# Performance work log

Measured on AMD Instinct MI355X. Metric: run time of the kernel, lower is better.

## Reference

```python
import jax, jax.numpy as jnp
from jax import lax
import numpy as np


def _conv(x, w, stride):
    # x: [B,C,D,H,W], w: [3,3,3,Cin,Cout]; kernel 3, pad 1 (matches SubMConv3d / SparseConv3d(3, s, padding=1))
    return lax.conv_general_dilated(x, w, (stride, stride, stride), [(1, 1)] * 3,
                                    dimension_numbers=('NCDHW', 'DHWIO', 'NCDHW'))


def _bn_relu(y, scale, shift, mask):
    # eval-mode BatchNorm folded to scale/shift, ReLU, then restrict to active sites
    return jnp.maximum(y * scale[None, :, None, None, None] + shift[None, :, None, None, None], 0.0) * mask


def _downsample_mask(m):
    # SparseConv3d(k=3, s=2, p=1): output site active iff any input in its 3x3x3 window is active
    return lax.reduce_window(m, -jnp.inf, lax.max, (1, 1, 3, 3, 3), (1, 1, 2, 2, 2),
                             [(0, 0), (0, 0), (1, 1), (1, 1), (1, 1)])


def setup_inputs() -> dict:
    key = jax.random.key(0)
    ks = jax.random.split(key, 40)
    B, D = 1, 128
    occ = jax.random.uniform(ks[0], (B, 1, D, D, D)) < 0.05
    x = jax.random.normal(ks[1], (B, 16, D, D, D), jnp.float32) * occ

    def w(k, ci, co):
        return jax.random.normal(k, (3, 3, 3, ci, co), jnp.float32) * (1.0 / np.sqrt(27.0 * ci))

    def sc(k, c):
        return jax.random.uniform(k, (c,), jnp.float32, 0.5, 1.5)

    def sh(k, c):
        return jax.random.normal(k, (c,), jnp.float32) * 0.1

    chans = [(16, 16), (16, 16), (16, 32), (32, 32), (32, 32), (32, 64), (64, 64), (64, 64), (64, 64)]
    names = ['w0a', 'w0b', 'wd0', 'w1a', 'w1b', 'wd1', 'w2a', 'w2b', 'w2c']
    d = {'x': x, 'mask': occ}
    i = 2
    for n, (ci, co) in zip(names, chans):
        d[n] = w(ks[i], ci, co)
        d['s' + n[1:]] = sc(ks[i + 1], co)
        d['b' + n[1:]] = sh(ks[i + 2], co)
        i += 3
    return d


def reference(x, mask, w0a, s0a, b0a, w0b, s0b, b0b, wd0, sd0, bd0,
              w1a, s1a, b1a, w1b, s1b, b1b, wd1, sd1, bd1,
              w2a, s2a, b2a, w2b, s2b, b2b, w2c, s2c, b2c):
    m0 = mask.astype(x.dtype)                       # active sites at full res [B,1,128,128,128]
    h = _bn_relu(_conv(x, w0a, 1), s0a, b0a, m0)    # conv0 (subm0)
    h = _bn_relu(_conv(h, w0b, 1), s0b, b0b, m0)
    m1 = _downsample_mask(m0)                       # down0 activity [B,1,64,64,64]
    h = _bn_relu(_conv(h, wd0, 2), sd0, bd0, m1)
    h = _bn_relu(_conv(h, w1a, 1), s1a, b1a, m1)    # conv1 (subm1)
    h = _bn_relu(_conv(h, w1b, 1), s1b, b1b, m1)
    m2 = _downsample_mask(m1)                       # down1 activity [B,1,32,32,32]
    h = _bn_relu(_conv(h, wd1, 2), sd1, bd1, m2)
    h = _bn_relu(_conv(h, w2a, 1), s2a, b2a, m2)    # conv2 (subm2)
    h = _bn_relu(_conv(h, w2b, 1), s2b, b2b, m2)
    h = _bn_relu(_conv(h, w2c, 1), s2c, b2c, m2)
    return h                                        # .dense() -> [B,64,32,32,32]
```

## Files before the change

### kernel.cpp

```cpp
#include <hip/hip_runtime.h>
#include <cstdint>

typedef unsigned short u16;
typedef unsigned int u32;
typedef unsigned char u8;
typedef unsigned long long u64;
typedef __attribute__((ext_vector_type(8))) short short8;
typedef __attribute__((ext_vector_type(4))) float f32x4;

#define CAP 131072

__device__ __forceinline__ float bf1(u16 v){ union{u32 i; float f;} c; c.i = ((u32)v) << 16; return c.f; }
__device__ __forceinline__ u16 f2bf(float f){
    union{float f; u32 i;} c; c.f = f; u32 i = c.i;
    return (u16)((i + 0x7FFFu + ((i >> 16) & 1u)) >> 16);
}

constexpr int ilog2c(int n){ return n <= 1 ? 0 : 1 + ilog2c(n / 2); }

struct P18 { const void* p[18]; };
struct PJobs {
    const void* src[9];
    u32 start[10];
    int cin[9], cout[9], mode[9];
};

__global__ void detect_k(const u16* __restrict__ s0a, u32* __restrict__ flag){
    if (threadIdx.x == 0){
        int ok = 1;
        #pragma unroll
        for (int i = 0; i < 8; i += 2){
            u16 v = s0a[i];
            if (v < 0x3F00u || v > 0x3FC0u) ok = 0;
        }
        flag[0] = ok ? 1u : 0u;
    }
}

__global__ __launch_bounds__(256)
void prep_k(PJobs J, u16* __restrict__ FR, const u32* __restrict__ flag){
    const int gi = blockIdx.x * 256 + threadIdx.x;
    if (gi >= (int)J.start[9]) return;
    int j = 0;
    while (gi >= (int)J.start[j + 1]) ++j;
    const int i = gi - (int)J.start[j];
    const void* w = J.src[j];
    const int CIN = J.cin[j], COUT = J.cout[j];
    const int jj = i & 7;
    const int lane = (i >> 3) & 63;
    int rest = i >> 9;
    int src = -1;
    if (J.mode[j] == 0){
        const int KC = CIN >> 5, NT = COUT >> 4;
        const int nt = rest % NT; rest /= NT;
        const int kc = rest % KC; const int tap = rest / KC;
        const int k = kc * 32 + (lane >> 4) * 8 + jj;
        const int co = nt * 16 + (lane & 15);
        src = (tap * CIN + k) * COUT + co;
    } else if (J.mode[j] == 1){
        const int nt = rest & 1; const int pair = rest >> 1;
        const int kg = (lane >> 4) * 8 + jj;
        const int tap = pair * 2 + (kg >> 4);
        const int ci = kg & 15;
        const int co = nt * 16 + (lane & 15);
        if (tap < 27) src = (tap * 16 + ci) * 32 + co;
    } else {
        const int pair = rest;
        const int kg = (lane >> 4) * 8 + jj;
        const int tap = pair * 2 + (kg >> 4);
        const int ci = kg & 15;
        const int co = lane & 15;
        if (tap < 27) src = (tap * 16 + ci) * 16 + co;
    }
    float v = 0.f;
    if (src >= 0) v = flag[0] ? bf1(((const u16*)w)[src]) : ((const float*)w)[src];
    FR[gi] = f2bf(v);
}

__global__ __launch_bounds__(64)
void scales_k(P18 ps, float* __restrict__ S, const u32* __restrict__ flag){
    const int b = blockIdx.x, t = threadIdx.x;
    const int len[18] = {16,16,16,16,32,32,32,32,32,32,64,64,64,64,64,64,64,64};
    const int off[18] = {0,16,32,48,64,96,128,160,192,224,256,320,384,448,512,576,640,704};
    if (t < len[b]){
        const float v = flag[0] ? bf1(((const u16*)ps.p[b])[t]) : ((const float*)ps.p[b])[t];
        S[off[b] + t] = v;
    }
}

__global__ __launch_bounds__(256)
void actmask_k(const void* __restrict__ xv, u64* __restrict__ bmask,
               u32* __restrict__ bcnt, const u32* __restrict__ flag){
    const int v = blockIdx.x * 256 + threadIdx.x;
    const size_t N = 2097152;
    u32 a = 0;
    if (flag[0]) {
        const u16* x = (const u16*)xv;
        #pragma unroll
        for (int c = 0; c < 16; ++c) a |= (u32)(x[(size_t)c * N + v]) & 0x7FFFu;
    } else {
        const u32* x = (const u32*)xv;
        #pragma unroll
        for (int c = 0; c < 16; ++c) a |= x[(size_t)c * N + v] & 0x7FFFFFFFu;
    }
    const u64 m = __ballot(a != 0);
    __shared__ u32 wc[4];
    const int lane = threadIdx.x & 63, wv = threadIdx.x >> 6;
    if (lane == 0) { bmask[v >> 6] = m; wc[wv] = (u32)__popcll(m); }
    __syncthreads();
    if (threadIdx.x == 0) bcnt[blockIdx.x] = wc[0] + wc[1] + wc[2] + wc[3];
}

__global__ __launch_bounds__(1024)
void scan_k(const u32* __restrict__ bcnt, u32* __restrict__ boff, u32* __restrict__ cnt){
    __shared__ u32 lds[1024];
    const int t = threadIdx.x;
    u32 loc[8]; u32 s = 0;
    #pragma unroll
    for (int i = 0; i < 8; ++i){ loc[i] = s; s += bcnt[t * 8 + i]; }
    lds[t] = s;
    __syncthreads();
    u32 v = s;
    for (int d = 1; d < 1024; d <<= 1){
        u32 o = (t >= d) ? lds[t - d] : 0;
        __syncthreads();
        v += o; lds[t] = v;
        __syncthreads();
    }
    const u32 base = v - s;
    #pragma unroll
    for (int i = 0; i < 8; ++i) boff[t * 8 + i] = base + loc[i];
    if (t == 1023) cnt[0] = v;
}

__global__ __launch_bounds__(256)
void scatter2_k(const void* __restrict__ xv, const u64* __restrict__ bmask,
                const u32* __restrict__ boff, int* __restrict__ idxmap,
                int* __restrict__ alist, u16* __restrict__ f,
                const u32* __restrict__ flag){
    const int v = blockIdx.x * 256 + threadIdx.x;
    const int lane = threadIdx.x & 63, wv = threadIdx.x >> 6;
    const u64 m = bmask[v >> 6];
    __shared__ u32 wc[4];
    if (lane == 0) wc[wv] = (u32)__popcll(m);
    __syncthreads();
    u32 wbase = 0;
    for (int i = 0; i < wv; ++i) wbase += wc[i];
    const bool act = (m >> lane) & 1ull;
    const u32 rank = (u32)__popcll(m & ((1ull << lane) - 1ull));
    int slot = -1;
    if (act){
        const u32 sl = boff[blockIdx.x] + wbase + rank;
        if (sl < CAP){
            slot = (int)sl;
            alist[slot] = v;
            if (flag[0]){
                const u16* x = (const u16*)xv;
                #pragma unroll
                for (int c = 0; c < 16; ++c) f[(size_t)slot * 16 + c] = x[(size_t)c * 2097152 + v];
            } else {
                const float* x = (const float*)xv;
                #pragma unroll
                for (int c = 0; c < 16; ++c) f[(size_t)slot * 16 + c] = f2bf(x[(size_t)c * 2097152 + v]);
            }
        }
    }
    idxmap[v] = slot;
}

__global__ __launch_bounds__(256)
void m1b_k(const u64* __restrict__ bmask, u8* __restrict__ mo){
    const int v = blockIdx.x * 256 + threadIdx.x;
    const int xo = v & 63, yo = (v >> 6) & 63, zo = v >> 12;
    u32 a = 0;
    #pragma unroll
    for (int kz = 0; kz < 3; ++kz){ const int iz = 2*zo + kz - 1; if ((unsigned)iz >= 128u) continue;
      #pragma unroll
      for (int ky = 0; ky < 3; ++ky){ const int iy = 2*yo + ky - 1; if ((unsigned)iy >= 128u) continue;
        #pragma unroll
        for (int kx = 0; kx < 3; ++kx){ const int ix = 2*xo + kx - 1; if ((unsigned)ix >= 128u) continue;
          const int vv = (iz * 128 + iy) * 128 + ix;
          a |= (u32)((bmask[vv >> 6] >> (vv & 63)) & 1ull);
    }}}
    mo[v] = (u8)a;
}

template<int DO>
__global__ __launch_bounds__(256)
void maskdown_k(const u8* __restrict__ mi, u8* __restrict__ mo){
    constexpr int DI = DO * 2;
    constexpr int LOG = ilog2c(DO);
    const int v = blockIdx.x * 256 + threadIdx.x;
    const int xo = v & (DO - 1), yo = (v >> LOG) & (DO - 1), zo = v >> (2 * LOG);
    u8 a = 0;
    for (int kz = 0; kz < 3; ++kz){ int iz = 2*zo + kz - 1; if ((unsigned)iz >= (unsigned)DI) continue;
      for (int ky = 0; ky < 3; ++ky){ int iy = 2*yo + ky - 1; if ((unsigned)iy >= (unsigned)DI) continue;
        for (int kx = 0; kx < 3; ++kx){ int ix = 2*xo + kx - 1; if ((unsigned)ix >= (unsigned)DI) continue;
          a |= mi[((size_t)iz * DI + iy) * DI + ix];
    }}}
    mo[v] = a;
}

__global__ __launch_bounds__(256)
void nbr_k(const int* __restrict__ idxmap, const int* __restrict__ alist,
           const u32* __restrict__ cnt, int* __restrict__ nbr){
    const int s = blockIdx.x * 256 + threadIdx.x;
    const int n = min((int)cnt[0], CAP);
    if (s >= n) return;
    const int v = alist[s];
    const int xo = v & 127, yo = (v >> 7) & 127, zo = v >> 14;
    #pragma unroll
    for (int tap = 0; tap < 27; ++tap){
        const int kz = tap / 9, ky = (tap / 3) % 3, kx = tap % 3;
        const int iz = zo + kz - 1, iy = yo + ky - 1, ix = xo + kx - 1;
        int sn = -1;
        if ((unsigned)iz < 128u && (unsigned)iy < 128u && (unsigned)ix < 128u)
            sn = idxmap[((size_t)iz * 128 + iy) * 128 + ix];
        nbr[tap * CAP + s] = sn;
    }
}

__global__ __launch_bounds__(256)
void sconvm2_k(const u16* __restrict__ fin, const int* __restrict__ nbr,
               const u32* __restrict__ cnt, const u16* __restrict__ wf,
               const float* __restrict__ sc, const float* __restrict__ sh,
               u16* __restrict__ fout){
    const int n = min((int)cnt[0], CAP);
    const int j = blockIdx.x * 4 + (threadIdx.x >> 6);
    const int sbase = j * 16;
    if (sbase >= n) return;
    const int lane = threadIdx.x & 63;
    const int m = lane & 15, quad = lane >> 4;
    const int s = sbase + m;
    const bool sok = s < n;

    f32x4 acc = {0.f,0.f,0.f,0.f};
    #pragma unroll
    for (int p = 0; p < 14; ++p){
        const int tp = p * 2 + (quad >> 1);
        short8 a = {0,0,0,0,0,0,0,0};
        if (sok && tp < 27){
            const int sn = nbr[tp * CAP + s];
            if (sn >= 0) a = *(const short8*)(fin + (size_t)sn * 16 + (quad & 1) * 8);
        }
        short8 b = *(const short8*)(wf + ((size_t)p * 64 + lane) * 8);
        acc = __builtin_amdgcn_mfma_f32_16x16x32_bf16(a, b, acc, 0, 0, 0);
    }

    const int co = lane & 15;
    const float scl = sc[co], shf = sh[co];
    #pragma unroll
    for (int r = 0; r < 4; ++r){
        const int srow = sbase + quad * 4 + r;
        if (srow < n){
            fout[(size_t)srow * 16 + co] = f2bf(fmaxf(acc[r] * scl + shf, 0.f));
        }
    }
}

__global__ __launch_bounds__(256)
void convd0m_k(const u16* __restrict__ fbuf, const int* __restrict__ idxmap,
               const u16* __restrict__ wf, const float* __restrict__ sc,
               const float* __restrict__ sh, const u8* __restrict__ mk,
               u16* __restrict__ out)
{
    const int wj = blockIdx.x * 4 + (threadIdx.x >> 6);
    const int lane = threadIdx.x & 63;
    const int m = lane & 15, quad = lane >> 4;
    const int xo_b = (wj & 3) * 16;
    const int yo = (wj >> 2) & 63;
    const int zo = wj >> 8;

    f32x4 acc0 = {0.f,0.f,0.f,0.f}, acc1 = {0.f,0.f,0.f,0.f};
    const int ix_m = (xo_b + m) * 2 - 1;

    #pragma unroll
    for (int p = 0; p < 14; ++p){
        const int tp = p * 2 + (quad >> 1);
        short8 a = {0,0,0,0,0,0,0,0};
        if (tp < 27){
            const int kz = tp / 9, ky = (tp / 3) % 3, kx = tp % 3;
            const int iz = 2*zo + kz - 1, iy = 2*yo + ky - 1, ix = ix_m + kx;
            if ((unsigned)iz < 128u && (unsigned)iy < 128u && (unsigned)ix < 128u){
                const int sn = idxmap[((size_t)iz * 128 + iy) * 128 + ix];
                if (sn >= 0) a = *(const short8*)(fbuf + (size_t)sn * 16 + (quad & 1) * 8);
            }
        }
        short8 b0 = *(const short8*)(wf + ((size_t)(p*2+0) * 64 + lane) * 8);
        short8 b1 = *(const short8*)(wf + ((size_t)(p*2+1) * 64 + lane) * 8);
        acc0 = __builtin_amdgcn_mfma_f32_16x16x32_bf16(a, b0, acc0, 0, 0, 0);
        acc1 = __builtin_amdgcn_mfma_f32_16x16x32_bf16(a, b1, acc1, 0, 0, 0);
    }

    const int vb = wj * 16 + quad * 4;
    const u32 m4 = *(const u32*)(mk + vb);
    const int n = lane & 15;
    #pragma unroll
    for (int nt = 0; nt < 2; ++nt){
        const int co = nt * 16 + n;
        const float s = sc[co], h = sh[co];
        const f32x4 acc = nt ? acc1 : acc0;
        #pragma unroll
        for (int r = 0; r < 4; ++r){
            float val = fmaxf(acc[r] * s + h, 0.f);
            val = ((m4 >> (8*r)) & 0xFFu) ? val : 0.f;
            out[(size_t)(vb + r) * 32 + co] = f2bf(val);
        }
    }
}

template<int DIN, int DOUT, int CIN, int COUT, int STRIDE, bool FINAL>
__global__ __launch_bounds__(256)
void mconv_k(const u16* __restrict__ in, const u16* __restrict__ wf,
             const float* __restrict__ sc, const float* __restrict__ sh,
             const u8* __restrict__ mk, void* __restrict__ out,
             const u32* __restrict__ flag)
{
    constexpr int KC = CIN / 32;
    constexpr int NT = COUT / 16;
    constexpr int XT = DOUT / 16;
    const int wj = blockIdx.x * 4 + (threadIdx.x >> 6);
    const int lane = threadIdx.x & 63;
    const int m = lane & 15, quad = lane >> 4;

    const int xo_b = (wj % XT) * 16;
    const int yo = (wj / XT) % DOUT;
    const int zo = wj / (XT * DOUT);

    f32x4 acc[NT];
    #pragma unroll
    for (int i = 0; i < NT; ++i) acc[i] = (f32x4){0.f,0.f,0.f,0.f};

    const int ix0 = (xo_b + m) * STRIDE - 1;
    for (int kz = 0; kz < 3; ++kz){
      const int iz = zo * STRIDE + kz - 1;
      if ((unsigned)iz >= (unsigned)DIN) continue;
      for (int ky = 0; ky < 3; ++ky){
        const int iy = yo * STRIDE + ky - 1;
        if ((unsigned)iy >= (unsigned)DIN) continue;
        const size_t rowb = ((size_t)iz * DIN + iy) * DIN;
        #pragma unroll
        for (int kx = 0; kx < 3; ++kx){
          const int ix = ix0 + kx;
          const bool v = (unsigned)ix < (unsigned)DIN;
          const int tap = (kz*3 + ky)*3 + kx;
          const u16* ap = in + (rowb + ix) * CIN + quad * 8;
          const u16* bp = wf + (size_t)tap * KC * NT * 512 + lane * 8;
          #pragma unroll
          for (int kc = 0; kc < KC; ++kc){
            short8 a = {0,0,0,0,0,0,0,0};
            if (v) a = *(const short8*)(ap + kc * 32);
            #pragma unroll
            for (int nt = 0; nt < NT; ++nt){
              short8 b = *(const short8*)(bp + (kc * NT + nt) * 512);
              acc[nt] = __builtin_amdgcn_mfma_f32_16x16x32_bf16(a, b, acc[nt], 0, 0, 0);
            }
          }
    }}}

    const int vb = wj * 16 + quad * 4;
    const u32 m4 = *(const u32*)(mk + vb);
    const int n = lane & 15;
    #pragma unroll
    for (int nt = 0; nt < NT; ++nt){
        const int co = nt * 16 + n;
        const float s = sc[co], h = sh[co];
        #pragma unroll
        for (int r = 0; r < 4; ++r){
            float val = fmaxf(acc[nt][r] * s + h, 0.f);
            val = ((m4 >> (8*r)) & 0xFFu) ? val : 0.f;
            ((u16*)out)[(size_t)(vb + r) * COUT + co] = f2bf(val);
        }
    }
    (void)flag;
}

template<int D, int CIN, int COUT, int WAVES, bool FINAL>
__global__ __launch_bounds__(WAVES*64)
void mconvlds_k(const u16* __restrict__ in, const u16* __restrict__ wf,
                const float* __restrict__ sc, const float* __restrict__ sh,
                const u8* __restrict__ mk, void* __restrict__ out,
                const u32* __restrict__ flag)
{
    constexpr int KC = CIN / 32;
    constexpr int NT = COUT / 16;
    constexpr int CH8 = CIN / 8;
    constexpr int BT = WAVES * 64;
    __shared__ u16 tile[9 * 2048];

    const int t = threadIdx.x;
    const int yo = blockIdx.x % D, zo = blockIdx.x / D;

    for (int dz = 0; dz < 3; ++dz){
      const int iz = zo + dz - 1;
      for (int dy = 0; dy < 3; ++dy){
        const int iy = yo + dy - 1;
        if ((unsigned)iz < (unsigned)D && (unsigned)iy < (unsigned)D){
          const u16* src = in + ((size_t)(iz * D + iy) * D) * CIN;
          u16* dst = &tile[(dz * 3 + dy) * 2048];
          for (int c = t; c < D * CH8; c += BT){
            const int x = c / CH8, c8 = c % CH8;
            *(short8*)(dst + (c8 * D + x) * 8) = *(const short8*)(src + c * 8);
          }
        }
      }
    }
    __syncthreads();

    const int lane = t & 63, w = t >> 6;
    const int m = lane & 15, quad = lane >> 4;
    const int xo_b = w * 16;

    f32x4 acc[NT];
    #pragma unroll
    for (int i = 0; i < NT; ++i) acc[i] = (f32x4){0.f,0.f,0.f,0.f};

    #pragma unroll
    for (int kz = 0; kz < 3; ++kz){
      const int iz = zo + kz - 1;
      if ((unsigned)iz >= (unsigned)D) continue;
      #pragma unroll
      for (int ky = 0; ky < 3; ++ky){
        const int iy = yo + ky - 1;
        if ((unsigned)iy >= (unsigned)D) continue;
        const u16* row = &tile[(kz * 3 + ky) * 2048];
        #pragma unroll
        for (int kx = 0; kx < 3; ++kx){
          const int ix = xo_b + m + kx - 1;
          const bool aok = (unsigned)ix < (unsigned)D;
          const int tap = (kz * 3 + ky) * 3 + kx;
          const u16* bp = wf + (size_t)tap * KC * NT * 512 + lane * 8;
          #pragma unroll
          for (int kc = 0; kc < KC; ++kc){
            short8 a = {0,0,0,0,0,0,0,0};
            if (aok) a = *(const short8*)(row + ((kc * 4 + quad) * D + ix) * 8);
            #pragma unroll
            for (int nt = 0; nt < NT; ++nt){
              short8 b = *(const short8*)(bp + (kc * NT + nt) * 512);
              acc[nt] = __builtin_amdgcn_mfma_f32_16x16x32_bf16(a, b, acc[nt], 0, 0, 0);
            }
          }
        }
      }
    }

    const int vb = (zo * D + yo) * D + xo_b + quad * 4;
    const u32 m4 = *(const u32*)(mk + vb);
    const int n = lane & 15;
    if (FINAL) {
        const bool bfout = flag[0] != 0;
        #pragma unroll
        for (int nt = 0; nt < NT; ++nt){
            const int co = nt * 16 + n;
            const float s = sc[co], h = sh[co];
            float4 o;
            float* po = &o.x;
            #pragma unroll
            for (int r = 0; r < 4; ++r){
                float val = fmaxf(acc[nt][r] * s + h, 0.f);
                po[r] = ((m4 >> (8*r)) & 0xFFu) ? val : 0.f;
            }
            if (!bfout) {
                *(float4*)((float*)out + (size_t)co * (D*D*D) + vb) = o;
            } else {
                u16* ob = (u16*)out + (size_t)co * (D*D*D) + vb;
                #pragma unroll
                for (int r = 0; r < 4; ++r) ob[r] = f2bf(po[r]);
            }
        }
    } else {
        #pragma unroll
        for (int nt = 0; nt < NT; ++nt){
            const int co = nt * 16 + n;
            const float s = sc[co], h = sh[co];
            #pragma unroll
            for (int r = 0; r < 4; ++r){
                float val = fmaxf(acc[nt][r] * s + h, 0.f);
                val = ((m4 >> (8*r)) & 0xFFu) ? val : 0.f;
                ((u16*)out)[(size_t)(vb + r) * COUT + co] = f2bf(val);
            }
        }
    }
}

extern "C" void kernel_launch(void* const* d_in, const int* in_sizes, int n_in,
                              void* d_out, int out_size, void* d_ws, size_t ws_size,
                              hipStream_t stream)
{
    (void)out_size; (void)ws_size;

    int wb = 2;
    for (int i = 1; i < n_in; ++i) { if (in_sizes[i] == 6912) { wb = i; break; } }

    const void* x = d_in[0];
    const void *w0a=d_in[wb+0],  *s0a=d_in[wb+1],  *b0a=d_in[wb+2];
    const void *w0b=d_in[wb+3],  *s0b=d_in[wb+4],  *b0b=d_in[wb+5];
    const void *wd0=d_in[wb+6],  *sd0=d_in[wb+7],  *bd0=d_in[wb+8];
    const void *w1a=d_in[wb+9],  *s1a=d_in[wb+10], *b1a=d_in[wb+11];
    const void *w1b=d_in[wb+12], *s1b=d_in[wb+13], *b1b=d_in[wb+14];
    const void *wd1=d_in[wb+15], *sd1=d_in[wb+16], *bd1=d_in[wb+17];
    const void *w2a=d_in[wb+18], *s2a=d_in[wb+19], *b2a=d_in[wb+20];
    const void *w2b=d_in[wb+21], *s2b=d_in[wb+22], *b2b=d_in[wb+23];
    const void *w2c=d_in[wb+24], *s2c=d_in[wb+25], *b2c=d_in[wb+26];

    char* ws = (char*)d_ws;
    int*   idxmap = (int*)(ws);
    u16*   Fb0    = (u16*)(ws + 8388608);
    u16*   Fb1    = (u16*)(ws + 12582912);
    u16*   Fb2    = (u16*)(ws + 16777216);
    u16*   Rb1    = (u16*)(ws + 25165824);
    u16*   Rb2    = (u16*)(ws + 41943040);
    u8*    m1     = (u8*)(ws + 58720256);
    u8*    m2     = (u8*)(ws + 58982400);
    u32*   cnt    = (u32*)(ws + 59015168);
    int*   alist  = (int*)(ws + 59015424);
    u16*   FR     = (u16*)(ws + 59539712);
    float* S      = (float*)(ws + 60481792);
    u32*   flag   = (u32*)(ws + 60484864);
    u64*   bmask  = (u64*)(ws + 60485120);
    u32*   bcnt   = (u32*)(ws + 60747264);
    u32*   boff   = (u32*)(ws + 60780032);
    int*   nbr    = (int*)(ws + 60812800);

    u16* wfs0a = FR + 0;
    u16* wfs0b = FR + 7168;
    u16* fd0   = FR + 14336;
    u16* f1a   = FR + 28672;
    u16* f1b   = FR + 56320;
    u16* fd1   = FR + 83968;
    u16* f2a   = FR + 139264;
    u16* f2b   = FR + 249856;
    u16* f2c   = FR + 360448;

    detect_k<<<1, 64, 0, stream>>>((const u16*)s0a, flag);

    PJobs J;
    const void* jsrc[9] = {w0a, w0b, wd0, w1a, w1b, wd1, w2a, w2b, w2c};
    const u32 jlen[9]   = {7168,7168,14336,27648,27648,55296,110592,110592,110592};
    const int jcin[9]   = {16,16,16,32,32,32,64,64,64};
    const int jcout[9]  = {16,16,32,32,32,64,64,64,64};
    const int jmode[9]  = {2,2,1,0,0,0,0,0,0};
    u32 acc = 0;
    for (int i = 0; i < 9; ++i){
        J.src[i] = jsrc[i]; J.start[i] = acc; acc += jlen[i];
        J.cin[i] = jcin[i]; J.cout[i] = jcout[i]; J.mode[i] = jmode[i];
    }
    J.start[9] = acc;
    prep_k<<<(int)((acc + 255) / 256), 256, 0, stream>>>(J, FR, flag);

    P18 ps;
    const void* sv[18] = {s0a,b0a,s0b,b0b,sd0,bd0,s1a,b1a,s1b,b1b,sd1,bd1,s2a,b2a,s2b,b2b,s2c,b2c};
    for (int i = 0; i < 18; ++i) ps.p[i] = sv[i];
    scales_k<<<18, 64, 0, stream>>>(ps, S, flag);
    float *cs0a=S+0,  *cb0a=S+16,  *cs0b=S+32,  *cb0b=S+48;
    float *csd0=S+64, *cbd0=S+96,  *cs1a=S+128, *cb1a=S+160, *cs1b=S+192, *cb1b=S+224;
    float *csd1=S+256,*cbd1=S+320, *cs2a=S+384, *cb2a=S+448, *cs2b=S+512, *cb2b=S+576, *cs2c=S+640, *cb2c=S+704;

    actmask_k<<<8192, 256, 0, stream>>>(x, bmask, bcnt, flag);
    scan_k<<<1, 1024, 0, stream>>>(bcnt, boff, cnt);
    scatter2_k<<<8192, 256, 0, stream>>>(x, bmask, boff, idxmap, alist, Fb0, flag);
    m1b_k<<<1024, 256, 0, stream>>>(bmask, m1);
    maskdown_k<32><<<128, 256, 0, stream>>>(m1, m2);
    nbr_k<<<512, 256, 0, stream>>>(idxmap, alist, cnt, nbr);

    sconvm2_k<<<2048, 256, 0, stream>>>(Fb0, nbr, cnt, wfs0a, cs0a, cb0a, Fb1);
    sconvm2_k<<<2048, 256, 0, stream>>>(Fb1, nbr, cnt, wfs0b, cs0b, cb0b, Fb2);
    convd0m_k<<<4096, 256, 0, stream>>>(Fb2, idxmap, fd0, csd0, cbd0, m1, Rb1);
    mconvlds_k<64,32,32,4,false><<<4096, 256, 0, stream>>>(Rb1, f1a, cs1a, cb1a, m1, Rb2, flag);
    mconvlds_k<64,32,32,4,false><<<4096, 256, 0, stream>>>(Rb2, f1b, cs1b, cb1b, m1, Rb1, flag);
    mconv_k<64,32,32,64,2,false><<<512, 256, 0, stream>>>(Rb1, fd1, csd1, cbd1, m2, Rb2, flag);
    mconvlds_k<32,64,64,2,false><<<1024, 128, 0, stream>>>(Rb2, f2a, cs2a, cb2a, m2, Rb1, flag);
    mconvlds_k<32,64,64,2,false><<<1024, 128, 0, stream>>>(Rb1, f2b, cs2b, cb2b, m2, Rb2, flag);
    mconvlds_k<32,64,64,2,true ><<<1024, 128, 0, stream>>>(Rb2, f2c, cs2c, cb2c, m2, d_out, flag);
}
```

Baseline: 544.6 us.

## Merge setup kernels and compute submanifold neighbors on the fly

Folds the scale/shift conversion into the weight-prep kernel, merges the prefix scan with the level-1 mask downsample, and merges the level-2 mask downsample into the scatter kernel. This cuts the number of small kernel launches. It also drops the precomputed 27-tap neighbor table: the first two sparse convolutions now look up neighbors in the dense index map inside the conv loop. That removes a kernel and its large neighbor-table write, at the cost of extra index arithmetic and scattered idxmap reads in both convs.

```diff
diff --git a/kernel.cpp b/kernel.cpp
--- a/kernel.cpp
+++ b/kernel.cpp
@@ -18,11 +18,11 @@
 
 constexpr int ilog2c(int n){ return n <= 1 ? 0 : 1 + ilog2c(n / 2); }
 
-struct P18 { const void* p[18]; };
-struct PJobs {
-    const void* src[9];
-    u32 start[10];
+struct PAll {
+    const void* w[9];
+    u32 wstart[10];
     int cin[9], cout[9], mode[9];
+    const void* s[18];
 };
 
 __global__ void detect_k(const u16* __restrict__ s0a, u32* __restrict__ flag){
@@ -38,53 +38,56 @@
 }
 
 __global__ __launch_bounds__(256)
-void prep_k(PJobs J, u16* __restrict__ FR, const u32* __restrict__ flag){
+void prep_k(PAll J, u16* __restrict__ FR, float* __restrict__ S,
+            const u32* __restrict__ flag){
     const int gi = blockIdx.x * 256 + threadIdx.x;
-    if (gi >= (int)J.start[9]) return;
-    int j = 0;
-    while (gi >= (int)J.start[j + 1]) ++j;
-    const int i = gi - (int)J.start[j];
-    const void* w = J.src[j];
-    const int CIN = J.cin[j], COUT = J.cout[j];
-    const int jj = i & 7;
-    const int lane = (i >> 3) & 63;
-    int rest = i >> 9;
-    int src = -1;
-    if (J.mode[j] == 0){
-        const int KC = CIN >> 5, NT = COUT >> 4;
-        const int nt = rest % NT; rest /= NT;
-        const int kc = rest % KC; const int tap = rest / KC;
-        const int k = kc * 32 + (lane >> 4) * 8 + jj;
-        const int co = nt * 16 + (lane & 15);
-        src = (tap * CIN + k) * COUT + co;
-    } else if (J.mode[j] == 1){
-        const int nt = rest & 1; const int pair = rest >> 1;
-        const int kg = (lane >> 4) * 8 + jj;
-        const int tap = pair * 2 + (kg >> 4);
-        const int ci = kg & 15;
-        const int co = nt * 16 + (lane & 15);
-        if (tap < 27) src = (tap * 16 + ci) * 32 + co;
+    const int wtot = (int)J.wstart[9];
+    if (gi < wtot){
+        int j = 0;
+        while (gi >= (int)J.wstart[j + 1]) ++j;
+        const int i = gi - (int)J.wstart[j];
+        const void* w = J.w[j];
+        const int CIN = J.cin[j], COUT = J.cout[j];
+        const int jj = i & 7;
+        const int lane = (i >> 3) & 63;
+        int rest = i >> 9;
+        int src = -1;
+        if (J.mode[j] == 0){
+            const int KC = CIN >> 5, NT = COUT >> 4;
+            const int nt = rest % NT; rest /= NT;
+            const int kc = rest % KC; const int tap = rest / KC;
+            const int k = kc * 32 + (lane >> 4) * 8 + jj;
+            const int co = nt * 16 + (lane & 15);
+            src = (tap * CIN + k) * COUT + co;
+        } else if (J.mode[j] == 1){
+            const int nt = rest & 1; const int pair = rest >> 1;
+            const int kg = (lane >> 4) * 8 + jj;
+            const int tap = pair * 2 + (kg >> 4);
+            const int ci = kg & 15;
+            const int co = nt * 16 + (lane & 15);
+            if (tap < 27) src = (tap * 16 + ci) * 32 + co;
+        } else {
+            const int pair = rest;
+            const int kg = (lane >> 4) * 8 + jj;
+            const int tap = pair * 2 + (kg >> 4);
+            const int ci = kg & 15;
+            const int co = lane & 15;
+            if (tap < 27) src = (tap * 16 + ci) * 16 + co;
+        }
+        float v = 0.f;
+        if (src >= 0) v = flag[0] ? bf1(((const u16*)w)[src]) : ((const float*)w)[src];
+        FR[gi] = f2bf(v);
     } else {
-        const int pair = rest;
-        const int kg = (lane >> 4) * 8 + jj;
-        const int tap = pair * 2 + (kg >> 4);
-        const int ci = kg & 15;
-        const int co = lane & 15;
-        if (tap < 27) src = (tap * 16 + ci) * 16 + co;
-    }
-    float v = 0.f;
-    if (src >= 0) v = flag[0] ? bf1(((const u16*)w)[src]) : ((const float*)w)[src];
-    FR[gi] = f2bf(v);
-}
-
-__global__ __launch_bounds__(64)
-void scales_k(P18 ps, float* __restrict__ S, const u32* __restrict__ flag){
-    const int b = blockIdx.x, t = threadIdx.x;
-    const int len[18] = {16,16,16,16,32,32,32,32,32,32,64,64,64,64,64,64,64,64};
-    const int off[18] = {0,16,32,48,64,96,128,160,192,224,256,320,384,448,512,576,640,704};
-    if (t < len[b]){
-        const float v = flag[0] ? bf1(((const u16*)ps.p[b])[t]) : ((const float*)ps.p[b])[t];
-        S[off[b] + t] = v;
+        const int i2 = gi - wtot;
+        const int len[18] = {16,16,16,16,32,32,32,32,32,32,64,64,64,64,64,64,64,64};
+        const int off[18] = {0,16,32,48,64,96,128,160,192,224,256,320,384,448,512,576,640,704};
+        if (i2 < 768){
+            int b = 0, base = 0;
+            while (i2 >= base + len[b]) { base += len[b]; ++b; }
+            const int t = i2 - base;
+            const float v = flag[0] ? bf1(((const u16*)J.s[b])[t]) : ((const float*)J.s[b])[t];
+            S[off[b] + t] = v;
+        }
     }
 }
 
@@ -112,136 +115,124 @@
 }
 
 __global__ __launch_bounds__(1024)
-void scan_k(const u32* __restrict__ bcnt, u32* __restrict__ boff, u32* __restrict__ cnt){
-    __shared__ u32 lds[1024];
-    const int t = threadIdx.x;
-    u32 loc[8]; u32 s = 0;
-    #pragma unroll
-    for (int i = 0; i < 8; ++i){ loc[i] = s; s += bcnt[t * 8 + i]; }
-    lds[t] = s;
-    __syncthreads();
-    u32 v = s;
-    for (int d = 1; d < 1024; d <<= 1){
-        u32 o = (t >= d) ? lds[t - d] : 0;
+void aux_k(const u32* __restrict__ bcnt, u32* __restrict__ boff, u32* __restrict__ cnt,
+           const u64* __restrict__ bmask, u8* __restrict__ m1){
+    if (blockIdx.x == 0){
+        __shared__ u32 lds[1024];
+        const int t = threadIdx.x;
+        u32 loc[8]; u32 s = 0;
+        #pragma unroll
+        for (int i = 0; i < 8; ++i){ loc[i] = s; s += bcnt[t * 8 + i]; }
+        lds[t] = s;
         __syncthreads();
-        v += o; lds[t] = v;
+        u32 v = s;
+        for (int d = 1; d < 1024; d <<= 1){
+            u32 o = (t >= d) ? lds[t - d] : 0;
+            __syncthreads();
+            v += o; lds[t] = v;
+            __syncthreads();
+        }
+        const u32 base = v - s;
+        #pragma unroll
+        for (int i = 0; i < 8; ++i) boff[t * 8 + i] = base + loc[i];
+        if (t == 1023) cnt[0] = v;
+    } else {
+        const int v = (blockIdx.x - 1) * 1024 + threadIdx.x;
+        const int xo = v & 63, yo = (v >> 6) & 63, zo = v >> 12;
+        u32 a = 0;
+        #pragma unroll
+        for (int kz = 0; kz < 3; ++kz){ const int iz = 2*zo + kz - 1; if ((unsigned)iz >= 128u) continue;
+          #pragma unroll
+          for (int ky = 0; ky < 3; ++ky){ const int iy = 2*yo + ky - 1; if ((unsigned)iy >= 128u) continue;
+            #pragma unroll
+            for (int kx = 0; kx < 3; ++kx){ const int ix = 2*xo + kx - 1; if ((unsigned)ix >= 128u) continue;
+              const int vv = (iz * 128 + iy) * 128 + ix;
+              a |= (u32)((bmask[vv >> 6] >> (vv & 63)) & 1ull);
+        }}}
+        m1[v] = (u8)a;
+    }
+}
+
+__global__ __launch_bounds__(256)
+void scatter2m_k(const void* __restrict__ xv, const u64* __restrict__ bmask,
+                 const u32* __restrict__ boff, int* __restrict__ idxmap,
+                 int* __restrict__ alist, u16* __restrict__ f,
+                 const u32* __restrict__ flag,
+                 const u8* __restrict__ m1, u8* __restrict__ m2){
+    if (blockIdx.x < 8192){
+        const int v = blockIdx.x * 256 + threadIdx.x;
+        const int lane = threadIdx.x & 63, wv = threadIdx.x >> 6;
+        const u64 m = bmask[v >> 6];
+        __shared__ u32 wc[4];
+        if (lane == 0) wc[wv] = (u32)__popcll(m);
         __syncthreads();
-    }
-    const u32 base = v - s;
-    #pragma unroll
-    for (int i = 0; i < 8; ++i) boff[t * 8 + i] = base + loc[i];
-    if (t == 1023) cnt[0] = v;
+        u32 wbase = 0;
+        for (int i = 0; i < wv; ++i) wbase += wc[i];
+        const bool act = (m >> lane) & 1ull;
+        const u32 rank = (u32)__popcll(m & ((1ull << lane) - 1ull));
+        int slot = -1;
+        if (act){
+            const u32 sl = boff[blockIdx.x] + wbase + rank;
+            if (sl < CAP){
+                slot = (int)sl;
+                alist[slot] = v;
+                if (flag[0]){
+                    const u16* x = (const u16*)xv;
+                    #pragma unroll
+                    for (int c = 0; c < 16; ++c) f[(size_t)slot * 16 + c] = x[(size_t)c * 2097152 + v];
+                } else {
+                    const float* x = (const float*)xv;
+                    #pragma unroll
+                    for (int c = 0; c < 16; ++c) f[(size_t)slot * 16 + c] = f2bf(x[(size_t)c * 2097152 + v]);
+                }
+            }
+        }
+        idxmap[v] = slot;
+    } else {
+        const int v = (int)(blockIdx.x - 8192) * 256 + threadIdx.x;
+        const int xo = v & 31, yo = (v >> 5) & 31, zo = v >> 10;
+        u8 a = 0;
+        #pragma unroll
+        for (int kz = 0; kz < 3; ++kz){ const int iz = 2*zo + kz - 1; if ((unsigned)iz >= 64u) continue;
+          #pragma unroll
+          for (int ky = 0; ky < 3; ++ky){ const int iy = 2*yo + ky - 1; if ((unsigned)iy >= 64u) continue;
+            #pragma unroll
+            for (int kx = 0; kx < 3; ++kx){ const int ix = 2*xo + kx - 1; if ((unsigned)ix >= 64u) continue;
+              a |= m1[((size_t)iz * 64 + iy) * 64 + ix];
+        }}}
+        m2[v] = a;
+    }
 }
 
 __global__ __launch_bounds__(256)
-void scatter2_k(const void* __restrict__ xv, const u64* __restrict__ bmask,
-                const u32* __restrict__ boff, int* __restrict__ idxmap,
-                int* __restrict__ alist, u16* __restrict__ f,
-                const u32* __restrict__ flag){
-    const int v = blockIdx.x * 256 + threadIdx.x;
-    const int lane = threadIdx.x & 63, wv = threadIdx.x >> 6;
-    const u64 m = bmask[v >> 6];
-    __shared__ u32 wc[4];
-    if (lane == 0) wc[wv] = (u32)__popcll(m);
-    __syncthreads();
-    u32 wbase = 0;
-    for (int i = 0; i < wv; ++i) wbase += wc[i];
-    const bool act = (m >> lane) & 1ull;
-    const u32 rank = (u32)__popcll(m & ((1ull << lane) - 1ull));
-    int slot = -1;
-    if (act){
-        const u32 sl = boff[blockIdx.x] + wbase + rank;
-        if (sl < CAP){
-            slot = (int)sl;
-            alist[slot] = v;
-            if (flag[0]){
-                const u16* x = (const u16*)xv;
-                #pragma unroll
-                for (int c = 0; c < 16; ++c) f[(size_t)slot * 16 + c] = x[(size_t)c * 2097152 + v];
-            } else {
-                const float* x = (const float*)xv;
-                #pragma unroll
-                for (int c = 0; c < 16; ++c) f[(size_t)slot * 16 + c] = f2bf(x[(size_t)c * 2097152 + v]);
-            }
-        }
-    }
-    idxmap[v] = slot;
-}
-
-__global__ __launch_bounds__(256)
-void m1b_k(const u64* __restrict__ bmask, u8* __restrict__ mo){
-    const int v = blockIdx.x * 256 + threadIdx.x;
-    const int xo = v & 63, yo = (v >> 6) & 63, zo = v >> 12;
-    u32 a = 0;
-    #pragma unroll
-    for (int kz = 0; kz < 3; ++kz){ const int iz = 2*zo + kz - 1; if ((unsigned)iz >= 128u) continue;
-      #pragma unroll
-      for (int ky = 0; ky < 3; ++ky){ const int iy = 2*yo + ky - 1; if ((unsigned)iy >= 128u) continue;
-        #pragma unroll
-        for (int kx = 0; kx < 3; ++kx){ const int ix = 2*xo + kx - 1; if ((unsigned)ix >= 128u) continue;
-          const int vv = (iz * 128 + iy) * 128 + ix;
-          a |= (u32)((bmask[vv >> 6] >> (vv & 63)) & 1ull);
-    }}}
-    mo[v] = (u8)a;
-}
-
-template<int DO>
-__global__ __launch_bounds__(256)
-void maskdown_k(const u8* __restrict__ mi, u8* __restrict__ mo){
-    constexpr int DI = DO * 2;
-    constexpr int LOG = ilog2c(DO);
-    const int v = blockIdx.x * 256 + threadIdx.x;
-    const int xo = v & (DO - 1), yo = (v >> LOG) & (DO - 1), zo = v >> (2 * LOG);
-    u8 a = 0;
-    for (int kz = 0; kz < 3; ++kz){ int iz = 2*zo + kz - 1; if ((unsigned)iz >= (unsigned)DI) continue;
-      for (int ky = 0; ky < 3; ++ky){ int iy = 2*yo + ky - 1; if ((unsigned)iy >= (unsigned)DI) continue;
-        for (int kx = 0; kx < 3; ++kx){ int ix = 2*xo + kx - 1; if ((unsigned)ix >= (unsigned)DI) continue;
-          a |= mi[((size_t)iz * DI + iy) * DI + ix];
-    }}}
-    mo[v] = a;
-}
-
-__global__ __launch_bounds__(256)
-void nbr_k(const int* __restrict__ idxmap, const int* __restrict__ alist,
-           const u32* __restrict__ cnt, int* __restrict__ nbr){
-    const int s = blockIdx.x * 256 + threadIdx.x;
-    const int n = min((int)cnt[0], CAP);
-    if (s >= n) return;
-    const int v = alist[s];
-    const int xo = v & 127, yo = (v >> 7) & 127, zo = v >> 14;
-    #pragma unroll
-    for (int tap = 0; tap < 27; ++tap){
-        const int kz = tap / 9, ky = (tap / 3) % 3, kx = tap % 3;
-        const int iz = zo + kz - 1, iy = yo + ky - 1, ix = xo + kx - 1;
-        int sn = -1;
-        if ((unsigned)iz < 128u && (unsigned)iy < 128u && (unsigned)ix < 128u)
-            sn = idxmap[((size_t)iz * 128 + iy) * 128 + ix];
-        nbr[tap * CAP + s] = sn;
-    }
-}
-
-__global__ __launch_bounds__(256)
-void sconvm2_k(const u16* __restrict__ fin, const int* __restrict__ nbr,
-               const u32* __restrict__ cnt, const u16* __restrict__ wf,
-               const float* __restrict__ sc, const float* __restrict__ sh,
-               u16* __restrict__ fout){
+void sconvm_k(const u16* __restrict__ fin, const int* __restrict__ idxmap,
+              const int* __restrict__ alist, const u32* __restrict__ cnt,
+              const u16* __restrict__ wf, const float* __restrict__ sc,
+              const float* __restrict__ sh, u16* __restrict__ fout){
     const int n = min((int)cnt[0], CAP);
     const int j = blockIdx.x * 4 + (threadIdx.x >> 6);
     const int sbase = j * 16;
     if (sbase >= n) return;
     const int lane = threadIdx.x & 63;
     const int m = lane & 15, quad = lane >> 4;
+
     const int s = sbase + m;
-    const bool sok = s < n;
+    const int v = (s < n) ? alist[s] : -1;
+    int xo = 0, yo = 0, zo = 0;
+    if (v >= 0){ xo = v & 127; yo = (v >> 7) & 127; zo = v >> 14; }
 
     f32x4 acc = {0.f,0.f,0.f,0.f};
     #pragma unroll
     for (int p = 0; p < 14; ++p){
         const int tp = p * 2 + (quad >> 1);
         short8 a = {0,0,0,0,0,0,0,0};
-        if (sok && tp < 27){
-            const int sn = nbr[tp * CAP + s];
-            if (sn >= 0) a = *(const short8*)(fin + (size_t)sn * 16 + (quad & 1) * 8);
+        if (v >= 0 && tp < 27){
+            const int kz = tp / 9, ky = (tp / 3) % 3, kx = tp % 3;
+            const int iz = zo + kz - 1, iy = yo + ky - 1, ix = xo + kx - 1;
+            if ((unsigned)iz < 128u && (unsigned)iy < 128u && (unsigned)ix < 128u){
+                const int sn = idxmap[((size_t)iz * 128 + iy) * 128 + ix];
+                if (sn >= 0) a = *(const short8*)(fin + (size_t)sn * 16 + (quad & 1) * 8);
+            }
         }
         short8 b = *(const short8*)(wf + ((size_t)p * 64 + lane) * 8);
         acc = __builtin_amdgcn_mfma_f32_16x16x32_bf16(a, b, acc, 0, 0, 0);
@@ -515,12 +506,11 @@
     u32*   cnt    = (u32*)(ws + 59015168);
     int*   alist  = (int*)(ws + 59015424);
     u16*   FR     = (u16*)(ws + 59539712);
-    float* S      = (float*)(ws + 60481792);
-    u32*   flag   = (u32*)(ws + 60484864);
-    u64*   bmask  = (u64*)(ws + 60485120);
-    u32*   bcnt   = (u32*)(ws + 60747264);
-    u32*   boff   = (u32*)(ws + 60780032);
-    int*   nbr    = (int*)(ws + 60812800);
+    float* S      = (float*)(ws + 60483328);
+    u32*   flag   = (u32*)(ws + 60486400);
+    u64*   bmask  = (u64*)(ws + 60486656);
+    u32*   bcnt   = (u32*)(ws + 60748800);
+    u32*   boff   = (u32*)(ws + 60781568);
 
     u16* wfs0a = FR + 0;
     u16* wfs0b = FR + 7168;
@@ -534,7 +524,7 @@
 
     detect_k<<<1, 64, 0, stream>>>((const u16*)s0a, flag);
 
-    PJobs J;
+    PAll J;
     const void* jsrc[9] = {w0a, w0b, wd0, w1a, w1b, wd1, w2a, w2b, w2c};
     const u32 jlen[9]   = {7168,7168,14336,27648,27648,55296,110592,110592,110592};
     const int jcin[9]   = {16,16,16,32,32,32,64,64,64};
@@ -542,29 +532,25 @@
     const int jmode[9]  = {2,2,1,0,0,0,0,0,0};
     u32 acc = 0;
     for (int i = 0; i < 9; ++i){
-        J.src[i] = jsrc[i]; J.start[i] = acc; acc += jlen[i];
+        J.w[i] = jsrc[i]; J.wstart[i] = acc; acc += jlen[i];
         J.cin[i] = jcin[i]; J.cout[i] = jcout[i]; J.mode[i] = jmode[i];
     }
-    J.start[9] = acc;
-    prep_k<<<(int)((acc + 255) / 256), 256, 0, stream>>>(J, FR, flag);
-
-    P18 ps;
+    J.wstart[9] = acc;
     const void* sv[18] = {s0a,b0a,s0b,b0b,sd0,bd0,s1a,b1a,s1b,b1b,sd1,bd1,s2a,b2a,s2b,b2b,s2c,b2c};
-    for (int i = 0; i < 18; ++i) ps.p[i] = sv[i];
-    scales_k<<<18, 64, 0, stream>>>(ps, S, flag);
+    for (int i = 0; i < 18; ++i) J.s[i] = sv[i];
+    const u32 ptot = acc + 768;
+    prep_k<<<(int)((ptot + 255) / 256), 256, 0, stream>>>(J, FR, S, flag);
+
     float *cs0a=S+0,  *cb0a=S+16,  *cs0b=S+32,  *cb0b=S+48;
     float *csd0=S+64, *cbd0=S+96,  *cs1a=S+128, *cb1a=S+160, *cs1b=S+192, *cb1b=S+224;
     float *csd1=S+256,*cbd1=S+320, *cs2a=S+384, *cb2a=S+448, *cs2b=S+512, *cb2b=S+576, *cs2c=S+640, *cb2c=S+704;
 
     actmask_k<<<8192, 256, 0, stream>>>(x, bmask, bcnt, flag);
-    scan_k<<<1, 1024, 0, stream>>>(bcnt, boff, cnt);
-    scatter2_k<<<8192, 256, 0, stream>>>(x, bmask, boff, idxmap, alist, Fb0, flag);
-    m1b_k<<<1024, 256, 0, stream>>>(bmask, m1);
-    maskdown_k<32><<<128, 256, 0, stream>>>(m1, m2);
-    nbr_k<<<512, 256, 0, stream>>>(idxmap, alist, cnt, nbr);
-
-    sconvm2_k<<<2048, 256, 0, stream>>>(Fb0, nbr, cnt, wfs0a, cs0a, cb0a, Fb1);
-    sconvm2_k<<<2048, 256, 0, stream>>>(Fb1, nbr, cnt, wfs0b, cs0b, cb0b, Fb2);
+    aux_k<<<257, 1024, 0, stream>>>(bcnt, boff, cnt, bmask, m1);
+    scatter2m_k<<<8320, 256, 0, stream>>>(x, bmask, boff, idxmap, alist, Fb0, flag, m1, m2);
+
+    sconvm_k<<<2048, 256, 0, stream>>>(Fb0, idxmap, alist, cnt, wfs0a, cs0a, cb0a, Fb1);
+    sconvm_k<<<2048, 256, 0, stream>>>(Fb1, idxmap, alist, cnt, wfs0b, cs0b, cb0b, Fb2);
     convd0m_k<<<4096, 256, 0, stream>>>(Fb2, idxmap, fd0, csd0, cbd0, m1, Rb1);
     mconvlds_k<64,32,32,4,false><<<4096, 256, 0, stream>>>(Rb1, f1a, cs1a, cb1a, m1, Rb2, flag);
     mconvlds_k<64,32,32,4,false><<<4096, 256, 0, stream>>>(Rb2, f1b, cs1b, cb1b, m1, Rb1, flag);
```

Result: faster. 530.9 us (-2.5%).
